# Kernel optimization log

Measured on AMD Instinct MI355X. Metric: run time of the kernel, lower is better.

## Reference

```python
import jax, jax.numpy as jnp
import numpy as np

N = 100000   # nodes
E = 1600000  # edges (avg degree 16)
D = 128      # embed_dim
H1, C1 = 8, 16   # gat1: heads=8, out=embed_dim//8=16, concat -> 128
C2 = 32          # gat2: heads=1, out=32
NEG_SLOPE = 0.2  # PyG GATConv default leaky relu slope


def _gat_layer(x, src, dst, W, a_src, a_dst, b, heads, ch, concat):
    """PyG-style GATConv (eval mode, add_self_loops already applied via src/dst)."""
    n = x.shape[0]
    h = (x @ W).reshape(n, heads, ch)                      # [N,H,C]
    alpha_s = jnp.einsum('nhc,hc->nh', h, a_src)           # [N,H]
    alpha_d = jnp.einsum('nhc,hc->nh', h, a_dst)           # [N,H]
    e = jax.nn.leaky_relu(alpha_s[src] + alpha_d[dst], NEG_SLOPE)  # [Etot,H]
    # segment softmax over incoming edges of each dst node
    m = jax.ops.segment_max(e, dst, num_segments=n)        # [N,H]
    ex = jnp.exp(e - m[dst])
    s = jax.ops.segment_sum(ex, dst, num_segments=n)       # [N,H]
    alpha = ex / (s[dst] + 1e-16)                          # [Etot,H]
    out = jax.ops.segment_sum(alpha[:, :, None] * h[src], dst, num_segments=n)  # [N,H,C]
    out = out.reshape(n, heads * ch) if concat else out.mean(axis=1)
    return out + b


def setup_inputs():
    key = jax.random.key(0)
    ks = jax.random.split(key, 12)
    x = jax.random.normal(ks[0], (N, D), dtype=jnp.float32)
    edge_index = jax.random.randint(ks[1], (2, E), 0, N, dtype=jnp.int64)
    sc = 0.1
    W1 = jax.random.normal(ks[2], (D, H1 * C1), jnp.float32) * sc
    a1_src = jax.random.normal(ks[3], (H1, C1), jnp.float32) * sc
    a1_dst = jax.random.normal(ks[4], (H1, C1), jnp.float32) * sc
    b1 = jnp.zeros((H1 * C1,), jnp.float32)
    W2 = jax.random.normal(ks[5], (H1 * C1, C2), jnp.float32) * sc
    a2_src = jax.random.normal(ks[6], (1, C2), jnp.float32) * sc
    a2_dst = jax.random.normal(ks[7], (1, C2), jnp.float32) * sc
    b2 = jnp.zeros((C2,), jnp.float32)
    Wh = jax.random.normal(ks[8], (C2, 1), jnp.float32) * sc
    bh = jnp.zeros((1,), jnp.float32)
    return {"x": x, "edge_index": edge_index,
            "W1": W1, "a1_src": a1_src, "a1_dst": a1_dst, "b1": b1,
            "W2": W2, "a2_src": a2_src, "a2_dst": a2_dst, "b2": b2,
            "Wh": Wh, "bh": bh}


def reference(x, edge_index, W1, a1_src, a1_dst, b1, W2, a2_src, a2_dst, b2, Wh, bh):
    n = x.shape[0]
    loops = jnp.arange(n, dtype=edge_index.dtype)
    src = jnp.concatenate([edge_index[0], loops])  # add_self_loops=True (PyG default)
    dst = jnp.concatenate([edge_index[1], loops])
    h = jax.nn.elu(_gat_layer(x, src, dst, W1, a1_src, a1_dst, b1, H1, C1, True))
    h = jax.nn.elu(_gat_layer(h, src, dst, W2, a2_src, a2_dst, b2, 1, C2, False))
    return h @ Wh + bh  # [N,1] ordinal head
```

## Files before the change

### kernel.cpp

```cpp
#include <hip/hip_runtime.h>
#include <hip/hip_bf16.h>
#include <stdint.h>
#include <stddef.h>

#define NEG_SLOPE 0.2f
#define XS 136

#define NBK   196
#define BWSH  9
#define BCAP  12288
#define NPREP 64

typedef __bf16 bf16x8 __attribute__((ext_vector_type(8)));
typedef float  f32x4  __attribute__((ext_vector_type(4)));

__device__ __forceinline__ float bf2f(__hip_bfloat16 b){ return __bfloat162float(b); }
__device__ __forceinline__ float lo_bf(unsigned u){ return __uint_as_float(u << 16); }
__device__ __forceinline__ float hi_bf(unsigned u){ return __uint_as_float(u & 0xffff0000u); }
__device__ __forceinline__ float lrelu(float u){ return fmaxf(u, NEG_SLOPE * u); }
__device__ __forceinline__ unsigned short f2bf(float f){
    unsigned u = __float_as_uint(f);
    return (unsigned short)((u + 0x7fffu + ((u >> 16) & 1u)) >> 16);
}
__device__ __forceinline__ float bfs2f(unsigned short s){ return __uint_as_float((unsigned)s << 16); }
__device__ __forceinline__ float ldraw(const void* p, int i, int isf){
    return isf ? ((const float*)p)[i] : bf2f(((const __hip_bfloat16*)p)[i]);
}

__global__ void detect_kernel(const unsigned* __restrict__ ei,
                              const unsigned* __restrict__ xw,
                              int* __restrict__ flags,
                              int* __restrict__ gcur){
    __shared__ int vote;
    const int t = threadIdx.x;
    if (t == 0) vote = 0;
    if (t < NBK) gcur[t] = t * BCAP;
    __syncthreads();
    if (t < 64){
        unsigned long long m = __ballot(ei[2*t + 1] != 0u);
        if (t == 0) flags[0] = (m == 0ull) ? 1 : 0;
    }
    {
        unsigned lo = xw[t] & 0xffffu;
        unsigned e  = (lo >> 7) & 0xffu;
        int pl = ((lo & 0x7fffu) == 0u || (e >= 100u && e <= 140u)) ? 1 : 0;
        atomicAdd(&vote, pl);
    }
    __syncthreads();
    if (t == 0) flags[1] = (vote < 128) ? 1 : 0;
}

#define WTS_TOTAL 20993
__global__ __launch_bounds__(256) void prep_scatter_kernel(
        const void* __restrict__ ei, const int* __restrict__ flags,
        int* __restrict__ gcur, unsigned* __restrict__ pairs, int E, int Et, int nsb,
        const void* W1, const void* W2, const void* a1s, const void* a1d,
        const void* b1, const void* a2s, const void* a2d, const void* b2,
        const void* Wh, const void* bh,
        float* __restrict__ w, unsigned short* __restrict__ w1x,
        unsigned short* __restrict__ w2x){
    const int t = threadIdx.x;
    if ((int)blockIdx.x < nsb){
        __shared__ int cnt[NBK], base[NBK], lcnt[NBK];
        const int e0 = blockIdx.x * 4096;
        const int nE = min(4096, Et - e0);
        for (int i = t; i < NBK; i += 256){ cnt[i] = 0; lcnt[i] = 0; }
        __syncthreads();
        const int is64 = flags[0];
        int2 sd[16];
#pragma unroll
        for (int k = 0; k < 16; k++){
            int j = t + k * 256;
            if (j < nE){
                int e = e0 + j, s, d;
                if (e >= E){ s = e - E; d = s; }
                else if (is64){
                    const long long* p = (const long long*)ei;
                    s = (int)p[e]; d = (int)p[(size_t)E + e];
                } else {
                    const int* p = (const int*)ei;
                    s = p[e]; d = p[(size_t)E + e];
                }
                sd[k] = make_int2(s, d);
                atomicAdd(&cnt[d >> BWSH], 1);
            } else sd[k].y = -1;
        }
        __syncthreads();
        for (int b = t; b < NBK; b += 256)
            base[b] = cnt[b] ? atomicAdd(&gcur[b], cnt[b]) : 0;
        __syncthreads();
#pragma unroll
        for (int k = 0; k < 16; k++){
            if (sd[k].y >= 0){
                int b = sd[k].y >> BWSH;
                int r = atomicAdd(&lcnt[b], 1);
                pairs[(size_t)base[b] + r] = ((unsigned)sd[k].x << BWSH) | (unsigned)(sd[k].y & 511);
            }
        }
    } else {
        const int p   = blockIdx.x - nsb;
        const int tid = p * 256 + t;
        const int NT  = NPREP * 256;
        const int isf = flags[1];
        for (int i = tid; i < 513; i += NT){
            int gi = 20480 + i;
            const void* src; int off;
            if      (gi < 20608){ src = a1s; off = gi - 20480; }
            else if (gi < 20736){ src = a1d; off = gi - 20608; }
            else if (gi < 20864){ src = b1;  off = gi - 20736; }
            else if (gi < 20896){ src = a2s; off = gi - 20864; }
            else if (gi < 20928){ src = a2d; off = gi - 20896; }
            else if (gi < 20960){ src = b2;  off = gi - 20928; }
            else if (gi < 20992){ src = Wh;  off = gi - 20960; }
            else                { src = bh;  off = 0; }
            w[gi] = ldraw(src, off, isf);
        }
        for (int i = tid; i < 16384; i += NT){
            int c = i >> 7, k = i & 127;
            w1x[i] = f2bf(ldraw(W1, k*128 + c, isf));
        }
        for (int i = tid; i < 4096; i += NT){
            int c = i >> 7, k = i & 127;
            w2x[i] = f2bf(ldraw(W2, k*32 + c, isf));
        }
        for (int i = tid; i < 12*128; i += NT) w2x[36*128 + i] = 0;
        for (int i = tid; i < 1024; i += NT){
            int h = i >> 7, k = i & 127;
            float ss = 0.f, dd = 0.f;
#pragma unroll
            for (int j = 0; j < 16; j++){
                float hv = ldraw(W1, k*128 + h*16 + j, isf);
                ss += hv * ldraw(a1s, h*16 + j, isf);
                dd += hv * ldraw(a1d, h*16 + j, isf);
            }
            unsigned short sh = f2bf(ss), dh = f2bf(dd);
            w1x[(128+h)*128 + k] = sh;
            w1x[(136+h)*128 + k] = f2bf(ss - bfs2f(sh));
            w1x[(144+h)*128 + k] = dh;
            w1x[(152+h)*128 + k] = f2bf(dd - bfs2f(dh));
        }
        for (int k = tid; k < 128; k += NT){
            float ss = 0.f, dd = 0.f;
#pragma unroll
            for (int j = 0; j < 32; j++){
                float hv = ldraw(W2, k*32 + j, isf);
                ss += hv * ldraw(a2s, j, isf);
                dd += hv * ldraw(a2d, j, isf);
            }
            unsigned short sh = f2bf(ss), dh = f2bf(dd);
            w2x[32*128 + k] = sh;
            w2x[33*128 + k] = f2bf(ss - bfs2f(sh));
            w2x[34*128 + k] = dh;
            w2x[35*128 + k] = f2bf(dd - bfs2f(dh));
        }
    }
}

__global__ __launch_bounds__(256) void g1csr_kernel(
        const unsigned* __restrict__ pairs, const int* __restrict__ gcur,
        int* __restrict__ rowptr, int* __restrict__ csr_src, int Nn,
        const void* __restrict__ xv, const unsigned short* __restrict__ w1x,
        const int* __restrict__ flags, __hip_bfloat16* __restrict__ h1b,
        float* __restrict__ as1, float* __restrict__ ad1){
    __shared__ __align__(16) char smem[52224];
    const int t = threadIdx.x;
    if ((int)blockIdx.x < NBK){
        int* ssz   = (int*)smem;
        int* sscan = ssz + 256;
        int* cnt   = sscan + 256;
        int* sh    = cnt + 512;
        const int b = blockIdx.x;
        int v = (t < NBK) ? (gcur[t] - t * BCAP) : 0;
        ssz[t] = v; sscan[t] = v;
        __syncthreads();
        for (int off = 1; off < 256; off <<= 1){
            int x = (t >= off) ? sscan[t - off] : 0;
            __syncthreads();
            sscan[t] += x;
            __syncthreads();
        }
        const int sz = ssz[b];
        const int eb = (b == 0) ? 0 : sscan[b - 1];
        if (b == 0 && t == 0) rowptr[Nn] = sscan[NBK - 1];
        const unsigned* pp = pairs + (size_t)b * BCAP;
        cnt[t] = 0; cnt[t + 256] = 0;
        __syncthreads();
        for (int i = t; i < sz; i += 256) atomicAdd(&cnt[pp[i] & 511u], 1);
        __syncthreads();
        int l0 = 2*t, l1 = 2*t + 1;
        int s0 = cnt[l0], s1 = cnt[l1], ts = s0 + s1;
        sh[t] = ts; __syncthreads();
        for (int off = 1; off < 256; off <<= 1){
            int x = (t >= off) ? sh[t - off] : 0;
            __syncthreads();
            sh[t] += x;
            __syncthreads();
        }
        int excl = sh[t] - ts;
        __syncthreads();
        cnt[l0] = eb + excl;
        cnt[l1] = eb + excl + s0;
        int n0 = (b << BWSH) + l0, n1 = (b << BWSH) + l1;
        if (n0 < Nn) rowptr[n0] = cnt[l0];
        if (n1 < Nn) rowptr[n1] = cnt[l1];
        __syncthreads();
        for (int i = t; i < sz; i += 256){
            unsigned sd = pp[i];
            int pos = atomicAdd(&cnt[sd & 511u], 1);
            csr_src[pos] = (int)(sd >> BWSH);
        }
    } else {
        __bf16* xls = (__bf16*)smem;
        __bf16* wls = (__bf16*)(smem + 64 * XS * 2);
        const int row0 = ((int)blockIdx.x - NBK) * 64;
        const int n = Nn;

#pragma unroll
        for (int k = 0; k < 8; k++){
            int e = (t + k * 256) * 8;
            int c = e >> 7, kk = e & 127;
            *(uint4*)(&wls[c * XS + kk]) = *(const uint4*)(w1x + e);
        }
        if (row0 + 64 <= n){
            if (flags[1]){
                const float* xp = (const float*)xv + (size_t)row0 * 128;
#pragma unroll
                for (int k = 0; k < 8; k++){
                    int e = (t + k * 256) * 4;
                    int row = e >> 7, col = e & 127;
                    float4 vv = *(const float4*)(xp + e);
                    uint2 o;
                    o.x = (unsigned)f2bf(vv.x) | ((unsigned)f2bf(vv.y) << 16);
                    o.y = (unsigned)f2bf(vv.z) | ((unsigned)f2bf(vv.w) << 16);
                    *(uint2*)(&xls[row * XS + col]) = o;
                }
            } else {
                const unsigned short* xp = (const unsigned short*)xv + (size_t)row0 * 128;
#pragma unroll
                for (int k = 0; k < 4; k++){
                    int e = (t + k * 256) * 8;
                    int row = e >> 7, col = e & 127;
                    *(uint4*)(&xls[row * XS + col]) = *(const uint4*)(xp + e);
                }
            }
        } else {
            const int limit = (n - row0) * 128;
            if (flags[1]){
                const float* xp = (const float*)xv + (size_t)row0 * 128;
                for (int i = t; i < 64 * 128; i += 256){
                    float v = (i < limit) ? xp[i] : 0.f;
                    xls[(i >> 7) * XS + (i & 127)] = (__bf16)v;
                }
            } else {
                const unsigned short* xp = (const unsigned short*)xv + (size_t)row0 * 128;
                for (int i = t; i < 64 * 128; i += 256){
                    unsigned short v = (i < limit) ? xp[i] : (unsigned short)0;
                    ((unsigned short*)xls)[(i >> 7) * XS + (i & 127)] = v;
                }
            }
        }
        __syncthreads();

        const int w    = t >> 6;
        const int lane = t & 63;
        const int l15  = lane & 15;
        const int quad = lane >> 4;

        f32x4 acc[8] = {};
        f32x4 accS = {}, accD = {};
        const __bf16* xbase = &xls[(w * 16 + l15) * XS + quad * 8];
        const __bf16* wbase = &wls[l15 * XS + quad * 8];
        const unsigned short* vsrow = w1x + (128 + l15) * 128 + quad * 8;
        const unsigned short* vdrow = w1x + (144 + l15) * 128 + quad * 8;

#pragma unroll
        for (int ks = 0; ks < 4; ks++){
            bf16x8 af = *(const bf16x8*)(xbase + ks * 32);
#pragma unroll
            for (int tt = 0; tt < 8; tt++){
                bf16x8 bfr = *(const bf16x8*)(wbase + tt * 16 * XS + ks * 32);
                acc[tt] = __builtin_amdgcn_mfma_f32_16x16x32_bf16(af, bfr, acc[tt], 0, 0, 0);
            }
            bf16x8 bS = *(const bf16x8*)(vsrow + ks * 32);
            bf16x8 bD = *(const bf16x8*)(vdrow + ks * 32);
            accS = __builtin_amdgcn_mfma_f32_16x16x32_bf16(af, bS, accS, 0, 0, 0);
            accD = __builtin_amdgcn_mfma_f32_16x16x32_bf16(af, bD, accD, 0, 0, 0);
        }

#pragma unroll
        for (int tt = 0; tt < 8; tt++){
            int col = tt * 16 + l15;
#pragma unroll
            for (int r = 0; r < 4; r++){
                int row = row0 + w * 16 + quad * 4 + r;
                if (row < n) h1b[(size_t)row * 128 + col] = __float2bfloat16(acc[tt][r]);
            }
        }
#pragma unroll
        for (int r = 0; r < 4; r++){
            float vs = accS[r] + __shfl_xor(accS[r], 8);
            float vd = accD[r] + __shfl_xor(accD[r], 8);
            int row = row0 + w * 16 + quad * 4 + r;
            if (l15 < 8 && row < n){
                as1[(size_t)row * 8 + l15] = vs;
                ad1[(size_t)row * 8 + l15] = vd;
            }
        }
    }
}

__global__ __launch_bounds__(256) void gather1_kernel(const int* __restrict__ rowptr,
                                                      const int* __restrict__ csr_src,
                                                      const float* __restrict__ as1,
                                                      const float* __restrict__ ad1,
                                                      const unsigned* __restrict__ h1u,
                                                      const float* __restrict__ b1,
                                                      unsigned* __restrict__ out1u, int n){
    int wid = blockIdx.x * 4 + (threadIdx.x >> 6);
    if (wid >= n) return;
    const int lane = threadIdx.x & 63;
    const int g    = lane >> 3;
    const int h    = lane & 7;
    const int start = rowptr[wid], end = rowptr[wid + 1];
    const float adv = ad1[(size_t)wid * 8 + h];
    float den = 0.f;
    float num[16] = {0.f,0.f,0.f,0.f,0.f,0.f,0.f,0.f,
                     0.f,0.f,0.f,0.f,0.f,0.f,0.f,0.f};
    int j   = start + g;
    int src = (j < end) ? csr_src[j] : -1;
    const int iters = (end - start + 7) >> 3;
#pragma unroll 2
    for (int it = 0; it < iters; ++it){
        const int jn   = j + 8;
        const int srcn = (jn < end) ? csr_src[jn] : -1;
        if (src >= 0){
            const unsigned* hp = h1u + (size_t)src * 64 + h * 8;
            uint4 hv0 = *(const uint4*)(hp);
            uint4 hv1 = *(const uint4*)(hp + 4);
            float u = lrelu(as1[src * 8 + h] + adv);
            float w = __expf(u);
            den += w;
            num[0]  += w * lo_bf(hv0.x); num[1]  += w * hi_bf(hv0.x);
            num[2]  += w * lo_bf(hv0.y); num[3]  += w * hi_bf(hv0.y);
            num[4]  += w * lo_bf(hv0.z); num[5]  += w * hi_bf(hv0.z);
            num[6]  += w * lo_bf(hv0.w); num[7]  += w * hi_bf(hv0.w);
            num[8]  += w * lo_bf(hv1.x); num[9]  += w * hi_bf(hv1.x);
            num[10] += w * lo_bf(hv1.y); num[11] += w * hi_bf(hv1.y);
            num[12] += w * lo_bf(hv1.z); num[13] += w * hi_bf(hv1.z);
            num[14] += w * lo_bf(hv1.w); num[15] += w * hi_bf(hv1.w);
        }
        j = jn; src = srcn;
    }
    den += __shfl_xor(den, 8); den += __shfl_xor(den, 16); den += __shfl_xor(den, 32);
#pragma unroll
    for (int k = 0; k < 16; k++){
        num[k] += __shfl_xor(num[k], 8);
        num[k] += __shfl_xor(num[k], 16);
        num[k] += __shfl_xor(num[k], 32);
    }
    if (g == 0){
        const int ch0 = h * 16;
        float inv = 1.f / (den + 1e-16f);
        uint4 o0, o1;
        unsigned* op0 = (unsigned*)&o0;
        unsigned* op1 = (unsigned*)&o1;
#pragma unroll
        for (int m = 0; m < 4; m++){
            float r0 = num[2*m]   * inv + b1[ch0 + 2*m];
            float r1 = num[2*m+1] * inv + b1[ch0 + 2*m + 1];
            r0 = r0 > 0.f ? r0 : __expf(r0) - 1.f;
            r1 = r1 > 0.f ? r1 : __expf(r1) - 1.f;
            op0[m] = (unsigned)f2bf(r0) | ((unsigned)f2bf(r1) << 16);
        }
#pragma unroll
        for (int m = 4; m < 8; m++){
            float r0 = num[2*m]   * inv + b1[ch0 + 2*m];
            float r1 = num[2*m+1] * inv + b1[ch0 + 2*m + 1];
            r0 = r0 > 0.f ? r0 : __expf(r0) - 1.f;
            r1 = r1 > 0.f ? r1 : __expf(r1) - 1.f;
            op1[m - 4] = (unsigned)f2bf(r0) | ((unsigned)f2bf(r1) << 16);
        }
        unsigned* ob = out1u + (size_t)wid * 64 + h * 8;
        *(uint4*)(ob)     = o0;
        *(uint4*)(ob + 4) = o1;
    }
}

__global__ __launch_bounds__(256) void gemm2_kernel(const unsigned* __restrict__ out1u,
                                                    const unsigned short* __restrict__ w2x,
                                                    __hip_bfloat16* __restrict__ h2b,
                                                    float* __restrict__ as2,
                                                    float* __restrict__ ad2, int n){
    __shared__ __align__(16) __bf16 als[64 * XS];
    __shared__ __align__(16) __bf16 wls[32 * XS];
    const int t = threadIdx.x;
    const int row0 = blockIdx.x * 64;

#pragma unroll
    for (int k = 0; k < 2; k++){
        int e = (t + k * 256) * 8;
        int c = e >> 7, kk = e & 127;
        *(uint4*)(&wls[c * XS + kk]) = *(const uint4*)(w2x + e);
    }
    if (row0 + 64 <= n){
#pragma unroll
        for (int k = 0; k < 4; k++){
            int e = (t + k * 256) * 4;
            int row = e >> 6, cu = e & 63;
            *(uint4*)(&((unsigned*)als)[row * 68 + cu]) =
                *(const uint4*)(out1u + (size_t)row0 * 64 + e);
        }
    } else {
        const int limit = (n - row0) * 64;
        for (int i = t; i < 64 * 64; i += 256){
            unsigned v = (i < limit) ? out1u[(size_t)row0 * 64 + i] : 0u;
            ((unsigned*)als)[(i >> 6) * 68 + (i & 63)] = v;
        }
    }
    __syncthreads();

    const int w    = t >> 6;
    const int lane = t & 63;
    const int l15  = lane & 15;
    const int quad = lane >> 4;

    f32x4 acc[2] = {};
    f32x4 accE = {};
    const __bf16* abase = &als[(w * 16 + l15) * XS + quad * 8];
    const __bf16* bbase = &wls[l15 * XS + quad * 8];
    const unsigned short* verow = w2x + (32 + l15) * 128 + quad * 8;

#pragma unroll
    for (int ks = 0; ks < 4; ks++){
        bf16x8 af = *(const bf16x8*)(abase + ks * 32);
#pragma unroll
        for (int tt = 0; tt < 2; tt++){
            bf16x8 bfr = *(const bf16x8*)(bbase + tt * 16 * XS + ks * 32);
            acc[tt] = __builtin_amdgcn_mfma_f32_16x16x32_bf16(af, bfr, acc[tt], 0, 0, 0);
        }
        bf16x8 bE = *(const bf16x8*)(verow + ks * 32);
        accE = __builtin_amdgcn_mfma_f32_16x16x32_bf16(af, bE, accE, 0, 0, 0);
    }

#pragma unroll
    for (int r = 0; r < 4; r++){
        int row = row0 + w * 16 + quad * 4 + r;
        if (row < n){
#pragma unroll
            for (int tt = 0; tt < 2; tt++){
                int col = tt * 16 + l15;
                h2b[(size_t)row * 32 + col] = __float2bfloat16(acc[tt][r]);
            }
        }
        float vE = accE[r] + __shfl_xor(accE[r], 1);
        if (row < n){
            if (l15 == 0) as2[row] = vE;
            if (l15 == 2) ad2[row] = vE;
        }
    }
}

__global__ __launch_bounds__(256) void gather2_kernel(const int* __restrict__ rowptr,
                                                      const int* __restrict__ csr_src,
                                                      const float* __restrict__ as2,
                                                      const float* __restrict__ ad2,
                                                      const unsigned* __restrict__ h2u,
                                                      const float* __restrict__ b2,
                                                      const float* __restrict__ Wh,
                                                      const float* __restrict__ bh,
                                                      const int* __restrict__ flags,
                                                      void* __restrict__ out, int n){
    int wid = blockIdx.x * 4 + (threadIdx.x >> 6);
    if (wid >= n) return;
    const int lane = threadIdx.x & 63;
    const int g = lane >> 2;
    const int c = lane & 3;
    const int start = rowptr[wid], end = rowptr[wid + 1];
    const float adv = ad2[wid];
    float den = 0.f;
    float num[8] = {0.f,0.f,0.f,0.f,0.f,0.f,0.f,0.f};
    int j   = start + g;
    int src = (j < end) ? csr_src[j] : -1;
    const int iters = (end - start + 15) >> 4;
#pragma unroll 2
    for (int it = 0; it < iters; ++it){
        const int jn   = j + 16;
        const int srcn = (jn < end) ? csr_src[jn] : -1;
        if (src >= 0){
            uint4 hv = *(const uint4*)(h2u + (size_t)src * 16 + c * 4);
            float u = lrelu(as2[src] + adv);
            float w = __expf(u);
            den += w;
            num[0] += w * lo_bf(hv.x); num[1] += w * hi_bf(hv.x);
            num[2] += w * lo_bf(hv.y); num[3] += w * hi_bf(hv.y);
            num[4] += w * lo_bf(hv.z); num[5] += w * hi_bf(hv.z);
            num[6] += w * lo_bf(hv.w); num[7] += w * hi_bf(hv.w);
        }
        j = jn; src = srcn;
    }
    den += __shfl_xor(den, 4); den += __shfl_xor(den, 8);
    den += __shfl_xor(den, 16); den += __shfl_xor(den, 32);
#pragma unroll
    for (int k = 0; k < 8; k++){
        num[k] += __shfl_xor(num[k], 4);
        num[k] += __shfl_xor(num[k], 8);
        num[k] += __shfl_xor(num[k], 16);
        num[k] += __shfl_xor(num[k], 32);
    }
    float p = 0.f;
    if (g == 0){
        const int ch0 = c * 8;
        float inv = 1.f / (den + 1e-16f);
#pragma unroll
        for (int k = 0; k < 8; k++){
            float v = num[k] * inv + b2[ch0 + k];
            v = v > 0.f ? v : __expf(v) - 1.f;
            p += v * Wh[ch0 + k];
        }
    }
    p += __shfl_xor(p, 1); p += __shfl_xor(p, 2);
    if (lane == 0){
        float r = p + bh[0];
        if (flags[1]) ((float*)out)[wid] = r;
        else          ((__hip_bfloat16*)out)[wid] = __float2bfloat16(r);
    }
}

extern "C" void kernel_launch(void* const* d_in, const int* in_sizes, int n_in,
                              void* d_out, int out_size, void* d_ws, size_t ws_size,
                              hipStream_t stream){
    const void* x   = d_in[0];
    const void* ei  = d_in[1];

    const int Nn = in_sizes[0] / 128;
    const int Ee = in_sizes[1] / 2;
    const int Et = Ee + Nn;
    const int nsb = (Et + 4095) / 4096;

    char* ws = (char*)d_ws;
    auto al = [](size_t v){ return (v + 255) & ~(size_t)255; };
    size_t off = 0;
    int*      flags  = (int*)(ws + off);      off = al(off + 16);
    float*    wts    = (float*)(ws + off);    off = al(off + (size_t)WTS_TOTAL * 4);
    unsigned short* w1x = (unsigned short*)(ws + off); off = al(off + 160 * 128 * 2);
    unsigned short* w2x = (unsigned short*)(ws + off); off = al(off + 48 * 128 * 2);
    int*      gcur   = (int*)(ws + off);      off = al(off + (size_t)NBK * 4);
    int*      rowptr = (int*)(ws + off);      off = al(off + (size_t)(Nn + 1) * 4);
    int*      csrs   = (int*)(ws + off);      off = al(off + (size_t)Et * 4);
    unsigned* pairs  = (unsigned*)(ws + off); off = al(off + (size_t)NBK * BCAP * 4);
    size_t o_h1 = off;
    __hip_bfloat16* h1b = (__hip_bfloat16*)(ws + off); off = al(off + (size_t)Nn * 128 * 2);
    float* as1  = (float*)(ws + off); off = al(off + (size_t)Nn * 8 * 4);
    float* ad1  = (float*)(ws + off); off = al(off + (size_t)Nn * 8 * 4);
    unsigned* out1u = (unsigned*)(ws + off); off = al(off + (size_t)Nn * 128 * 2);
    size_t o2 = o_h1;
    __hip_bfloat16* h2b = (__hip_bfloat16*)(ws + o2); o2 += (size_t)Nn * 32 * 2;
    float* as2  = (float*)(ws + o2);  o2 += (size_t)Nn * 4;
    float* ad2  = (float*)(ws + o2);  o2 += (size_t)Nn * 4;

    float* b1f  = wts + 20736;
    float* b2f  = wts + 20928;
    float* Whf  = wts + 20960;
    float* bhf  = wts + 20992;

    detect_kernel<<<1, 256, 0, stream>>>((const unsigned*)ei, (const unsigned*)x, flags, gcur);

    prep_scatter_kernel<<<nsb + NPREP, 256, 0, stream>>>(ei, flags, gcur, pairs, Ee, Et, nsb,
        d_in[2], d_in[6], d_in[3], d_in[4], d_in[5], d_in[7], d_in[8], d_in[9],
        d_in[10], d_in[11], wts, w1x, w2x);

    g1csr_kernel<<<NBK + (Nn + 63) / 64, 256, 0, stream>>>(pairs, gcur, rowptr, csrs, Nn,
        x, w1x, flags, h1b, as1, ad1);

    gather1_kernel<<<(Nn + 3) / 4, 256, 0, stream>>>(rowptr, csrs, as1, ad1,
                                                     (const unsigned*)h1b, b1f, out1u, Nn);

    gemm2_kernel<<<(Nn + 63) / 64, 256, 0, stream>>>(out1u, w2x, h2b, as2, ad2, Nn);

    gather2_kernel<<<(Nn + 3) / 4, 256, 0, stream>>>(rowptr, csrs, as2, ad2,
                                                     (const unsigned*)h2b, b2f,
                                                     Whf, bhf, flags, d_out, Nn);
}
```

Measured before the change: 296.6 us.

## Store layer-1 features head-major and split gather1 into per-head passes

The layer-1 GEMM now writes h1 and the attention logits in a head-major layout, so each head's features form a contiguous [N,16] slab. The gather kernel launches eight times as many blocks, one group per head, and each wave handles one destination node for one head with 16 edges in flight and 4 channels per lane. The goal is to shrink the working set each gather pass touches (a 3.2MB slab per head instead of the full feature matrix) so random source reads hit cache better. It also adds nontemporal loads and stores. The cost is that the CSR indices and row pointers are reread eight times, and each node's output is written as eight partial 8-byte stores.

After: 519.0 us. 1.75x slower.

```diff
diff --git a/kernel.cpp b/kernel.cpp
--- a/kernel.cpp
+++ b/kernel.cpp
@@ -289,11 +289,11 @@
 
 #pragma unroll
         for (int tt = 0; tt < 8; tt++){
-            int col = tt * 16 + l15;
 #pragma unroll
             for (int r = 0; r < 4; r++){
                 int row = row0 + w * 16 + quad * 4 + r;
-                if (row < n) h1b[(size_t)row * 128 + col] = __float2bfloat16(acc[tt][r]);
+                if (row < n)
+                    h1b[((size_t)tt * n + row) * 16 + l15] = __float2bfloat16(acc[tt][r]);
             }
         }
 #pragma unroll
@@ -302,8 +302,8 @@
             float vd = accD[r] + __shfl_xor(accD[r], 8);
             int row = row0 + w * 16 + quad * 4 + r;
             if (l15 < 8 && row < n){
-                as1[(size_t)row * 8 + l15] = vs;
-                ad1[(size_t)row * 8 + l15] = vd;
+                as1[(size_t)l15 * n + row] = vs;
+                ad1[(size_t)l15 * n + row] = vd;
             }
         }
     }
@@ -315,74 +315,62 @@
                                                       const float* __restrict__ ad1,
                                                       const unsigned* __restrict__ h1u,
                                                       const float* __restrict__ b1,
-                                                      unsigned* __restrict__ out1u, int n){
-    int wid = blockIdx.x * 4 + (threadIdx.x >> 6);
+                                                      unsigned* __restrict__ out1u,
+                                                      int n, int nbph){
+    const int h   = blockIdx.x / nbph;
+    const int wid = (blockIdx.x % nbph) * 4 + (threadIdx.x >> 6);
     if (wid >= n) return;
     const int lane = threadIdx.x & 63;
-    const int g    = lane >> 3;
-    const int h    = lane & 7;
+    const int g = lane >> 2;
+    const int c = lane & 3;
     const int start = rowptr[wid], end = rowptr[wid + 1];
-    const float adv = ad1[(size_t)wid * 8 + h];
+    const float* ash = as1 + (size_t)h * n;
+    const unsigned* hh = h1u + (size_t)h * n * 8;
+    const float adv = ad1[(size_t)h * n + wid];
     float den = 0.f;
-    float num[16] = {0.f,0.f,0.f,0.f,0.f,0.f,0.f,0.f,
-                     0.f,0.f,0.f,0.f,0.f,0.f,0.f,0.f};
+    float num[4] = {0.f,0.f,0.f,0.f};
     int j   = start + g;
-    int src = (j < end) ? csr_src[j] : -1;
-    const int iters = (end - start + 7) >> 3;
+    int src = (j < end) ? __builtin_nontemporal_load(csr_src + j) : -1;
+    const int iters = (end - start + 15) >> 4;
 #pragma unroll 2
     for (int it = 0; it < iters; ++it){
-        const int jn   = j + 8;
-        const int srcn = (jn < end) ? csr_src[jn] : -1;
+        const int jn   = j + 16;
+        const int srcn = (jn < end) ? __builtin_nontemporal_load(csr_src + jn) : -1;
         if (src >= 0){
-            const unsigned* hp = h1u + (size_t)src * 64 + h * 8;
-            uint4 hv0 = *(const uint4*)(hp);
-            uint4 hv1 = *(const uint4*)(hp + 4);
-            float u = lrelu(as1[src * 8 + h] + adv);
+            uint2 hv = *(const uint2*)(hh + (size_t)src * 8 + c * 2);
+            float u = lrelu(ash[src] + adv);
             float w = __expf(u);
             den += w;
-            num[0]  += w * lo_bf(hv0.x); num[1]  += w * hi_bf(hv0.x);
-            num[2]  += w * lo_bf(hv0.y); num[3]  += w * hi_bf(hv0.y);
-            num[4]  += w * lo_bf(hv0.z); num[5]  += w * hi_bf(hv0.z);
-            num[6]  += w * lo_bf(hv0.w); num[7]  += w * hi_bf(hv0.w);
-            num[8]  += w * lo_bf(hv1.x); num[9]  += w * hi_bf(hv1.x);
-            num[10] += w * lo_bf(hv1.y); num[11] += w * hi_bf(hv1.y);
-            num[12] += w * lo_bf(hv1.z); num[13] += w * hi_bf(hv1.z);
-            num[14] += w * lo_bf(hv1.w); num[15] += w * hi_bf(hv1.w);
+            num[0] += w * lo_bf(hv.x); num[1] += w * hi_bf(hv.x);
+            num[2] += w * lo_bf(hv.y); num[3] += w * hi_bf(hv.y);
         }
         j = jn; src = srcn;
     }
-    den += __shfl_xor(den, 8); den += __shfl_xor(den, 16); den += __shfl_xor(den, 32);
-#pragma unroll
-    for (int k = 0; k < 16; k++){
+    den += __shfl_xor(den, 4);  den += __shfl_xor(den, 8);
+    den += __shfl_xor(den, 16); den += __shfl_xor(den, 32);
+#pragma unroll
+    for (int k = 0; k < 4; k++){
+        num[k] += __shfl_xor(num[k], 4);
         num[k] += __shfl_xor(num[k], 8);
         num[k] += __shfl_xor(num[k], 16);
         num[k] += __shfl_xor(num[k], 32);
     }
     if (g == 0){
-        const int ch0 = h * 16;
+        const int ch0 = h * 16 + c * 4;
         float inv = 1.f / (den + 1e-16f);
-        uint4 o0, o1;
-        unsigned* op0 = (unsigned*)&o0;
-        unsigned* op1 = (unsigned*)&o1;
-#pragma unroll
-        for (int m = 0; m < 4; m++){
-            float r0 = num[2*m]   * inv + b1[ch0 + 2*m];
-            float r1 = num[2*m+1] * inv + b1[ch0 + 2*m + 1];
-            r0 = r0 > 0.f ? r0 : __expf(r0) - 1.f;
-            r1 = r1 > 0.f ? r1 : __expf(r1) - 1.f;
-            op0[m] = (unsigned)f2bf(r0) | ((unsigned)f2bf(r1) << 16);
-        }
-#pragma unroll
-        for (int m = 4; m < 8; m++){
-            float r0 = num[2*m]   * inv + b1[ch0 + 2*m];
-            float r1 = num[2*m+1] * inv + b1[ch0 + 2*m + 1];
-            r0 = r0 > 0.f ? r0 : __expf(r0) - 1.f;
-            r1 = r1 > 0.f ? r1 : __expf(r1) - 1.f;
-            op1[m - 4] = (unsigned)f2bf(r0) | ((unsigned)f2bf(r1) << 16);
-        }
-        unsigned* ob = out1u + (size_t)wid * 64 + h * 8;
-        *(uint4*)(ob)     = o0;
-        *(uint4*)(ob + 4) = o1;
+        float r0 = num[0] * inv + b1[ch0 + 0];
+        float r1 = num[1] * inv + b1[ch0 + 1];
+        float r2 = num[2] * inv + b1[ch0 + 2];
+        float r3 = num[3] * inv + b1[ch0 + 3];
+        r0 = r0 > 0.f ? r0 : __expf(r0) - 1.f;
+        r1 = r1 > 0.f ? r1 : __expf(r1) - 1.f;
+        r2 = r2 > 0.f ? r2 : __expf(r2) - 1.f;
+        r3 = r3 > 0.f ? r3 : __expf(r3) - 1.f;
+        unsigned lo32 = (unsigned)f2bf(r0) | ((unsigned)f2bf(r1) << 16);
+        unsigned hi32 = (unsigned)f2bf(r2) | ((unsigned)f2bf(r3) << 16);
+        unsigned long long o = (unsigned long long)lo32 | ((unsigned long long)hi32 << 32);
+        __builtin_nontemporal_store(o,
+            (unsigned long long*)(out1u + (size_t)wid * 64 + h * 8 + c * 2));
     }
 }
 
@@ -572,8 +560,9 @@
     g1csr_kernel<<<NBK + (Nn + 63) / 64, 256, 0, stream>>>(pairs, gcur, rowptr, csrs, Nn,
         x, w1x, flags, h1b, as1, ad1);
 
-    gather1_kernel<<<(Nn + 3) / 4, 256, 0, stream>>>(rowptr, csrs, as1, ad1,
-                                                     (const unsigned*)h1b, b1f, out1u, Nn);
+    const int nbph = (Nn + 3) / 4;
+    gather1_kernel<<<8 * nbph, 256, 0, stream>>>(rowptr, csrs, as1, ad1,
+                                                 (const unsigned*)h1b, b1f, out1u, Nn, nbph);
 
     gemm2_kernel<<<(Nn + 63) / 64, 256, 0, stream>>>(out1u, w2x, h2b, as2, ad2, Nn);
 
```

## Stage bucketed edge pairs in LDS for coalesced writes; nontemporal CSR loads

Applied to the files above, without the earlier changes.

The edge-bucketing scatter now ranks each edge within its bucket using the first atomic pass, prefix-scans the bucket counts, and stages the packed pairs contiguously in shared memory. It then writes each bucket's run to global memory with one wave per bucket, giving coalesced stores in place of scattered per-edge stores. gcur now holds a count relative to each bucket's base instead of an absolute offset. The gather kernels also read csr_src with nontemporal loads to keep the streamed index array from displacing reused feature rows in cache. The cost is an extra 16 KB of LDS per block, a block-wide scan, and more barriers.

New measurement: 303.2 us. 2.3% more time.

```diff
diff --git a/kernel.cpp b/kernel.cpp
--- a/kernel.cpp
+++ b/kernel.cpp
@@ -34,7 +34,7 @@
     __shared__ int vote;
     const int t = threadIdx.x;
     if (t == 0) vote = 0;
-    if (t < NBK) gcur[t] = t * BCAP;
+    if (t < NBK) gcur[t] = 0;
     __syncthreads();
     if (t < 64){
         unsigned long long m = __ballot(ei[2*t + 1] != 0u);
@@ -61,13 +61,17 @@
         unsigned short* __restrict__ w2x){
     const int t = threadIdx.x;
     if ((int)blockIdx.x < nsb){
-        __shared__ int cnt[NBK], base[NBK], lcnt[NBK];
+        __shared__ int cnt[256];
+        __shared__ int scn[256];
+        __shared__ int base[NBK];
+        __shared__ unsigned stage[4096];
+        cnt[t] = 0;
+        __syncthreads();
+        const int is64 = flags[0];
         const int e0 = blockIdx.x * 4096;
         const int nE = min(4096, Et - e0);
-        for (int i = t; i < NBK; i += 256){ cnt[i] = 0; lcnt[i] = 0; }
-        __syncthreads();
-        const int is64 = flags[0];
         int2 sd[16];
+        int  rk[16];
 #pragma unroll
         for (int k = 0; k < 16; k++){
             int j = t + k * 256;
@@ -82,20 +86,37 @@
                     s = p[e]; d = p[(size_t)E + e];
                 }
                 sd[k] = make_int2(s, d);
-                atomicAdd(&cnt[d >> BWSH], 1);
+                rk[k] = atomicAdd(&cnt[d >> BWSH], 1);
             } else sd[k].y = -1;
         }
         __syncthreads();
-        for (int b = t; b < NBK; b += 256)
-            base[b] = cnt[b] ? atomicAdd(&gcur[b], cnt[b]) : 0;
+        int v = cnt[t];
+        scn[t] = v;
+        __syncthreads();
+        for (int off = 1; off < 256; off <<= 1){
+            int x = (t >= off) ? scn[t - off] : 0;
+            __syncthreads();
+            scn[t] += x;
+            __syncthreads();
+        }
+        if (t < NBK) base[t] = cnt[t] ? atomicAdd(&gcur[t], cnt[t]) : 0;
         __syncthreads();
 #pragma unroll
         for (int k = 0; k < 16; k++){
             if (sd[k].y >= 0){
                 int b = sd[k].y >> BWSH;
-                int r = atomicAdd(&lcnt[b], 1);
-                pairs[(size_t)base[b] + r] = ((unsigned)sd[k].x << BWSH) | (unsigned)(sd[k].y & 511);
-            }
+                stage[(scn[b] - cnt[b]) + rk[k]] =
+                    ((unsigned)sd[k].x << BWSH) | (unsigned)(sd[k].y & 511);
+            }
+        }
+        __syncthreads();
+        const int wv = t >> 6, lane = t & 63;
+        for (int b = wv; b < NBK; b += 4){
+            const int c  = cnt[b];
+            const int sb = scn[b] - c;
+            unsigned* gp = pairs + (size_t)b * BCAP + base[b];
+            const unsigned* sp = stage + sb;
+            for (int i = lane; i < c; i += 64) gp[i] = sp[i];
         }
     } else {
         const int p   = blockIdx.x - nsb;
@@ -170,7 +191,7 @@
         int* cnt   = sscan + 256;
         int* sh    = cnt + 512;
         const int b = blockIdx.x;
-        int v = (t < NBK) ? (gcur[t] - t * BCAP) : 0;
+        int v = (t < NBK) ? gcur[t] : 0;
         ssz[t] = v; sscan[t] = v;
         __syncthreads();
         for (int off = 1; off < 256; off <<= 1){
@@ -327,12 +348,12 @@
     float num[16] = {0.f,0.f,0.f,0.f,0.f,0.f,0.f,0.f,
                      0.f,0.f,0.f,0.f,0.f,0.f,0.f,0.f};
     int j   = start + g;
-    int src = (j < end) ? csr_src[j] : -1;
+    int src = (j < end) ? __builtin_nontemporal_load(csr_src + j) : -1;
     const int iters = (end - start + 7) >> 3;
 #pragma unroll 2
     for (int it = 0; it < iters; ++it){
         const int jn   = j + 8;
-        const int srcn = (jn < end) ? csr_src[jn] : -1;
+        const int srcn = (jn < end) ? __builtin_nontemporal_load(csr_src + jn) : -1;
         if (src >= 0){
             const unsigned* hp = h1u + (size_t)src * 64 + h * 8;
             uint4 hv0 = *(const uint4*)(hp);
@@ -480,12 +501,12 @@
     float den = 0.f;
     float num[8] = {0.f,0.f,0.f,0.f,0.f,0.f,0.f,0.f};
     int j   = start + g;
-    int src = (j < end) ? csr_src[j] : -1;
+    int src = (j < end) ? __builtin_nontemporal_load(csr_src + j) : -1;
     const int iters = (end - start + 15) >> 4;
 #pragma unroll 2
     for (int it = 0; it < iters; ++it){
         const int jn   = j + 16;
-        const int srcn = (jn < end) ? csr_src[jn] : -1;
+        const int srcn = (jn < end) ? __builtin_nontemporal_load(csr_src + jn) : -1;
         if (src >= 0){
             uint4 hv = *(const uint4*)(h2u + (size_t)src * 16 + c * 4);
             float u = lrelu(as2[src] + adv);
```
